# Kernel optimization log

Hardware: AMD Instinct MI355X
Metric: run time of the kernel (lower is better)

## Reference

```python
import jax, jax.numpy as jnp
import numpy as np
import math

B, L, D, H = 4, 4096, 1024, 16
d = D // H

def setup_inputs() -> dict:
    key = jax.random.key(0)
    ks = jax.random.split(key, 8)
    s = 0.02
    x = jax.random.normal(ks[0], (B, L, D), dtype=jnp.float32)
    Wqkv_w = jax.random.normal(ks[1], (3 * D, D), dtype=jnp.float32) * s
    Wqkv_b = jnp.zeros((3 * D,), dtype=jnp.float32)
    out_w = jax.random.normal(ks[2], (D, D), dtype=jnp.float32) * s
    out_b = jnp.zeros((D,), dtype=jnp.float32)
    W_static = jax.random.normal(ks[3], (H, d, d), dtype=jnp.float32) * s
    Lambda_raw = jax.random.uniform(ks[4], (H, d, d), dtype=jnp.float32, minval=-3.0, maxval=3.0)
    g = 0.5 / math.sqrt(d)
    Gamma = jax.random.uniform(ks[5], (H, d, d), dtype=jnp.float32, minval=-g, maxval=g)
    return {"x": x, "Wqkv_w": Wqkv_w, "Wqkv_b": Wqkv_b, "out_w": out_w,
            "out_b": out_b, "W_static": W_static, "Lambda_raw": Lambda_raw, "Gamma": Gamma}

def _stp_forward(x, Wqkv_w, Wqkv_b, out_w, out_b, W_static, Lambda_raw, Gamma):
    b, l, dm = x.shape
    scale = 1.0 / math.sqrt(d)
    qkv = x @ Wqkv_w.T + Wqkv_b                      # (B,L,3D)
    qkv = qkv.reshape(b, l, 3, H, d)                 # 'b l (three h d)'
    qkv = jnp.transpose(qkv, (2, 0, 3, 1, 4))        # (3,B,H,L,d)
    q, k, v = qkv[0], qkv[1], qkv[2]
    k = k * scale
    retention = 1.0 - jax.nn.sigmoid(Lambda_raw)     # (H,d,d)

    # scan over time: carry state (B,H,d,d)
    qs = jnp.moveaxis(q, 2, 0)                       # (L,B,H,d)
    ks_ = jnp.moveaxis(k, 2, 0)
    vs = jnp.moveaxis(v, 2, 0)

    def step(state, qkv_t):
        q_t, k_t, v_t = qkv_t                        # each (B,H,d)
        hebbian = jnp.einsum('bhi,bhj->bhij', v_t, k_t)
        state = retention[None] * state + Gamma[None] * hebbian
        y_t = jnp.einsum('bhij,bhj->bhi', W_static[None] + state, q_t)
        return state, y_t

    state0 = jnp.zeros((b, H, d, d), dtype=x.dtype)
    _, ys = jax.lax.scan(step, state0, (qs, ks_, vs))  # ys: (L,B,H,d)
    y = jnp.transpose(ys, (1, 0, 2, 3)).reshape(b, l, dm)  # 'b h l d -> b l (h d)'
    return y @ out_w.T + out_b

def reference(x, Wqkv_w, Wqkv_b, out_w, out_b, W_static, Lambda_raw, Gamma):
    return _stp_forward(x, Wqkv_w, Wqkv_b, out_w, out_b, W_static, Lambda_raw, Gamma)
```

## Files before the change

### kernel.cpp

```cpp
#include <hip/hip_runtime.h>
#include <stdint.h>

typedef unsigned short u16;
typedef __bf16 bf16x8 __attribute__((ext_vector_type(8)));
typedef float  f32x4  __attribute__((ext_vector_type(4)));

#define GLOBAL_AS __attribute__((address_space(1)))
#define LDS_AS    __attribute__((address_space(3)))

#define B_ 4
#define L_ 4096
#define D_ 1024
#define H_ 16
#define TD 3072

__device__ __forceinline__ float bf2f(u16 h) {
    union { uint32_t u; float f; } v; v.u = ((uint32_t)h) << 16; return v.f;
}
__device__ __forceinline__ u16 f2bf(float f) {
    union { float f; uint32_t u; } v; v.f = f;
    uint32_t u = v.u;
    u += 0x7fffu + ((u >> 16) & 1u);
    return (u16)(u >> 16);
}
__device__ __forceinline__ void unp2(uint32_t u, float* f) {
    union { uint32_t u; float f; } lo, hi;
    lo.u = u << 16; hi.u = u & 0xffff0000u;
    f[0] = lo.f; f[1] = hi.f;
}
__device__ __forceinline__ void unp8(uint4 u, float* f) {
    unp2(u.x, f); unp2(u.y, f + 2); unp2(u.z, f + 4); unp2(u.w, f + 6);
}

#define DPP_STEP(N)                                                           \
    {                                                                         \
        union { float f; int i; } s_, a_;                                     \
        a_.f = x;                                                             \
        s_.i = __builtin_amdgcn_update_dpp(0, a_.i, 0x110 + N, 0xf, 0xf, true); \
        x += s_.f;                                                            \
    }
__device__ __forceinline__ float grp_sum8(float x) {
    DPP_STEP(1) DPP_STEP(2) DPP_STEP(4)
    return x;
}

__device__ __forceinline__ uint4 ld8f(const float* p) {
    const float4 a = *(const float4*)p;
    const float4 b = *(const float4*)(p + 4);
    uint4 r;
    r.x = (uint32_t)f2bf(a.x) | ((uint32_t)f2bf(a.y) << 16);
    r.y = (uint32_t)f2bf(a.z) | ((uint32_t)f2bf(a.w) << 16);
    r.z = (uint32_t)f2bf(b.x) | ((uint32_t)f2bf(b.y) << 16);
    r.w = (uint32_t)f2bf(b.z) | ((uint32_t)f2bf(b.w) << 16);
    return r;
}

__device__ __forceinline__ void stc(u16* p, float v)   { *p = f2bf(v); }
__device__ __forceinline__ void stc(float* p, float v) { *p = v; }

__global__ __launch_bounds__(256) void cvt_f32_bf16(
    const float* __restrict__ in, u16* __restrict__ out, size_t n8)
{
    size_t i = (size_t)blockIdx.x * 256 + threadIdx.x;
    if (i >= n8) return;
    *(uint4*)(out + i * 8) = ld8f(in + i * 8);
}

template <typename TC>
__global__ __launch_bounds__(256) void gemm_bt_bias_bf16(
    const u16* __restrict__ A, const u16* __restrict__ W,
    const float* __restrict__ bias, TC* __restrict__ C,
    int M, int N, int K)
{
    __shared__ u16 As[128 * 32];
    __shared__ u16 Bs[128 * 32];

    const int tid  = threadIdx.x;
    const int lane = tid & 63;
    const int wid  = tid >> 6;
    const int bm = blockIdx.y * 128;
    const int bn = blockIdx.x * 128;

    const int wm = (wid & 1) * 64;
    const int wn = (wid >> 1) * 64;
    const int fr   = lane & 15;
    const int quad = lane >> 4;

    const u16* Ag = A + (size_t)(bm + (tid >> 2)) * K + (tid & 3) * 8;
    const u16* Wg = W + (size_t)(bn + (tid >> 2)) * K + (tid & 3) * 8;
    const size_t rskip = (size_t)64 * K;

    u16* AsW = As + wid * 512;
    u16* BsW = Bs + wid * 512;

    f32x4 acc[4][4] = {};

    for (int k0 = 0; k0 < K; k0 += 32) {
        __syncthreads();
        __builtin_amdgcn_global_load_lds((const GLOBAL_AS void*)(Ag + k0),
                                         (LDS_AS void*)(AsW),        16, 0, 0);
        __builtin_amdgcn_global_load_lds((const GLOBAL_AS void*)(Ag + rskip + k0),
                                         (LDS_AS void*)(AsW + 2048), 16, 0, 0);
        __builtin_amdgcn_global_load_lds((const GLOBAL_AS void*)(Wg + k0),
                                         (LDS_AS void*)(BsW),        16, 0, 0);
        __builtin_amdgcn_global_load_lds((const GLOBAL_AS void*)(Wg + rskip + k0),
                                         (LDS_AS void*)(BsW + 2048), 16, 0, 0);
        __syncthreads();

        bf16x8 af[4], bfv[4];
#pragma unroll
        for (int tm = 0; tm < 4; ++tm) {
            int m = wm + tm * 16 + fr;
            af[tm] = *(const bf16x8*)&As[m * 32 + quad * 8];
        }
#pragma unroll
        for (int tn = 0; tn < 4; ++tn) {
            int n = wn + tn * 16 + fr;
            bfv[tn] = *(const bf16x8*)&Bs[n * 32 + quad * 8];
        }
#pragma unroll
        for (int tm = 0; tm < 4; ++tm)
#pragma unroll
            for (int tn = 0; tn < 4; ++tn)
                acc[tm][tn] = __builtin_amdgcn_mfma_f32_16x16x32_bf16(
                    af[tm], bfv[tn], acc[tm][tn], 0, 0, 0);
    }

#pragma unroll
    for (int tm = 0; tm < 4; ++tm) {
#pragma unroll
        for (int tn = 0; tn < 4; ++tn) {
            const int col = bn + wn + tn * 16 + fr;
            const float bv = bias[col];
#pragma unroll
            for (int r = 0; r < 4; ++r) {
                const int row = bm + wm + tm * 16 + quad * 4 + r;
                stc(&C[(size_t)row * N + col], acc[tm][tn][r] + bv);
            }
        }
    }
}

__global__ __launch_bounds__(256, 4) void stp_scan_local(
    const u16* __restrict__ qkv, const float* __restrict__ Lam,
    const float* __restrict__ Gam, float* __restrict__ F,
    int nchunk, int tchunk)
{
    const int c = blockIdx.x, h = blockIdx.y, b = blockIdx.z;
    const int t = threadIdx.x;
    const int ig = t >> 3, jc = t & 7;
    const int i0 = ig << 1, j0 = jc << 3;
    const int hij = (h << 12) + (i0 << 6) + j0;

    float R2[2][8], RG[2][8], G[2][8], s[2][8];
#pragma unroll
    for (int r = 0; r < 2; ++r)
#pragma unroll
        for (int j = 0; j < 8; ++j) {
            const float Rv = 1.0f / (1.0f + expf(Lam[hij + r * 64 + j]));
            const float Gv = Gam[hij + r * 64 + j] * 0.125f;
            R2[r][j] = Rv * Rv;
            RG[r][j] = Rv * Gv;
            G[r][j]  = Gv;
            s[r][j]  = 0.0f;
        }

    const u16* rowp = qkv + (size_t)(b * L_ + c * tchunk) * TD;
    const int koff = D_ + (h << 6) + j0;
    const int voff = 2 * D_ + (h << 6) + i0;

    uint4    k0 = *(const uint4*)(rowp + koff);
    uint4    k1 = *(const uint4*)(rowp + TD + koff);
    uint32_t v0 = *(const uint32_t*)(rowp + voff);
    uint32_t v1 = *(const uint32_t*)(rowp + TD + voff);

    for (int tt = 0; tt < tchunk; tt += 2) {
        uint4    k0n = *(const uint4*)(rowp + 2 * TD + koff);
        uint4    k1n = *(const uint4*)(rowp + 3 * TD + koff);
        uint32_t v0n = *(const uint32_t*)(rowp + 2 * TD + voff);
        uint32_t v1n = *(const uint32_t*)(rowp + 3 * TD + voff);

        float kf0[8], kf1[8];
        unp8(k0, kf0); unp8(k1, kf1);
        const float a0 = bf2f((u16)v0), a1 = bf2f((u16)(v0 >> 16));
        const float b0 = bf2f((u16)v1), b1 = bf2f((u16)(v1 >> 16));
#pragma unroll
        for (int j = 0; j < 8; ++j) {
            s[0][j] = fmaf(R2[0][j], s[0][j],
                           fmaf(G[0][j], b0 * kf1[j], RG[0][j] * (a0 * kf0[j])));
            s[1][j] = fmaf(R2[1][j], s[1][j],
                           fmaf(G[1][j], b1 * kf1[j], RG[1][j] * (a1 * kf0[j])));
        }
        k0 = k0n; k1 = k1n; v0 = v0n; v1 = v1n;
        rowp += 2 * TD;
    }

    float* Fp = F + (((size_t)(b * H_ + h) * nchunk + c) << 12) + (i0 << 6) + j0;
#pragma unroll
    for (int r = 0; r < 2; ++r) {
        *(f32x4*)(Fp + r * 64)     = *(const f32x4*)(&s[r][0]);
        *(f32x4*)(Fp + r * 64 + 4) = *(const f32x4*)(&s[r][4]);
    }
}

__global__ __launch_bounds__(256) void stp_combine(
    const float* __restrict__ Lam, float* __restrict__ F,
    int nchunk, int tchunk)
{
    const int h = blockIdx.x, b = blockIdx.y;
    const int t = threadIdx.x;
    const int i = t >> 2, jc = t & 3, j0 = jc << 4;
    const int hij = (h << 12) + (i << 6) + j0;

    float Rt[16], s[16];
#pragma unroll
    for (int j = 0; j < 16; ++j) {
        float R = 1.0f / (1.0f + expf(Lam[hij + j]));
        Rt[j] = powf(R, (float)tchunk);
        s[j] = 0.0f;
    }
    float* base = F + (((size_t)(b * H_ + h) * nchunk) << 12) + (i << 6) + j0;
    for (int c = 0; c < nchunk; ++c) {
        float* p = base + ((size_t)c << 12);
        float tmp[16];
#pragma unroll
        for (int j = 0; j < 16; ++j) tmp[j] = p[j];
#pragma unroll
        for (int j = 0; j < 16; ++j) { p[j] = s[j]; s[j] = fmaf(Rt[j], s[j], tmp[j]); }
    }
}

__global__ __launch_bounds__(256, 4) void stp_scan_out(
    const u16* __restrict__ qkv, const float* __restrict__ Lam,
    const float* __restrict__ Gam, const float* __restrict__ Wst,
    const float* __restrict__ Sinit, u16* __restrict__ y,
    int nchunk, int tchunk)
{
    const int c = blockIdx.x, h = blockIdx.y, b = blockIdx.z;
    const int t = threadIdx.x;
    const int ig = t >> 3, jc = t & 7;
    const int i0 = ig << 1, j0 = jc << 3;
    const int hij = (h << 12) + (i0 << 6) + j0;

    float R[2][8], Gv[2][8], Cc[2][8], s[2][8];
    const float* Sp = Sinit + (((size_t)(b * H_ + h) * nchunk + c) << 12) + (i0 << 6) + j0;
#pragma unroll
    for (int r = 0; r < 2; ++r)
#pragma unroll
        for (int j = 0; j < 8; ++j) {
            const float Rv = 1.0f / (1.0f + expf(Lam[hij + r * 64 + j]));
            const float Wv = Wst[hij + r * 64 + j];
            R[r][j]  = Rv;
            Gv[r][j] = Gam[hij + r * 64 + j] * 0.125f;
            Cc[r][j] = Wv * (1.0f - Rv);
            s[r][j]  = Sp[r * 64 + j] + Wv;
        }

    const u16* rowp = qkv + (size_t)(b * L_ + c * tchunk) * TD;
    const int qoff = (h << 6) + j0;
    const int koff = D_ + qoff;
    const int voff = 2 * D_ + (h << 6) + i0;
    u16* yp = y + (size_t)(b * L_ + c * tchunk) * D_ + (h << 6) + i0;

    uint4    qu = *(const uint4*)(rowp + qoff);
    uint4    ku = *(const uint4*)(rowp + koff);
    uint32_t vu = *(const uint32_t*)(rowp + voff);

    for (int tt = 0; tt < tchunk; ++tt) {
        uint4    qn = *(const uint4*)(rowp + TD + qoff);
        uint4    kn = *(const uint4*)(rowp + TD + koff);
        uint32_t vn = *(const uint32_t*)(rowp + TD + voff);

        float qf[8], kf[8];
        unp8(qu, qf); unp8(ku, kf);
        const float v0 = bf2f((u16)vu);
        const float v1 = bf2f((u16)(vu >> 16));

        float ya0 = 0.0f, ya1 = 0.0f;
#pragma unroll
        for (int j = 0; j < 8; ++j) {
            s[0][j] = fmaf(R[0][j], s[0][j], fmaf(Gv[0][j] * v0, kf[j], Cc[0][j]));
            ya0 = fmaf(s[0][j], qf[j], ya0);
            s[1][j] = fmaf(R[1][j], s[1][j], fmaf(Gv[1][j] * v1, kf[j], Cc[1][j]));
            ya1 = fmaf(s[1][j], qf[j], ya1);
        }
        ya0 = grp_sum8(ya0);
        ya1 = grp_sum8(ya1);
        if ((t & 7) == 7) {
            uint32_t pk = (uint32_t)f2bf(ya0) | ((uint32_t)f2bf(ya1) << 16);
            *(uint32_t*)yp = pk;
        }
        qu = qn; ku = kn; vu = vn;
        rowp += TD; yp += D_;
    }
}

__global__ void zero_out_f32(float* p, size_t n) {
    size_t i = (size_t)blockIdx.x * blockDim.x + threadIdx.x;
    if (i < n) p[i] = 0.0f;
}

extern "C" void kernel_launch(void* const* d_in, const int* in_sizes, int n_in,
                              void* d_out, int out_size, void* d_ws, size_t ws_size,
                              hipStream_t stream)
{
    const float* x      = (const float*)d_in[0];
    const float* Wqkv_w = (const float*)d_in[1];
    const float* Wqkv_b = (const float*)d_in[2];
    const float* out_w  = (const float*)d_in[3];
    const float* out_b  = (const float*)d_in[4];
    const float* Wst    = (const float*)d_in[5];
    const float* Lam    = (const float*)d_in[6];
    const float* Gam    = (const float*)d_in[7];
    float* out = (float*)d_out;

    const size_t qkv_e = (size_t)B_ * L_ * TD;
    const size_t y_e   = (size_t)B_ * L_ * D_;
    const size_t fixed = qkv_e * 2 + y_e * 2;

    int nchunk = 32;
    size_t fbytes = (size_t)B_ * H_ * nchunk * 64 * 64 * 4;
    if (ws_size < fixed + fbytes) {
        nchunk = 16;
        fbytes = (size_t)B_ * H_ * nchunk * 64 * 64 * 4;
    }
    if (ws_size < fixed + fbytes) {
        zero_out_f32<<<(out_size + 255) / 256, 256, 0, stream>>>(out, (size_t)out_size);
        return;
    }
    const int tchunk = L_ / nchunk;

    u16*   qkv = (u16*)d_ws;
    u16*   y   = qkv + qkv_e;
    float* F   = (float*)(y + y_e);
    u16*   xb    = y;
    u16*   wqkvb = (u16*)F;
    u16*   outwb = (u16*)F;

    cvt_f32_bf16<<<(B_ * L_ * D_ / 8 + 255) / 256, 256, 0, stream>>>(
        x, xb, (size_t)B_ * L_ * D_ / 8);
    cvt_f32_bf16<<<(TD * D_ / 8 + 255) / 256, 256, 0, stream>>>(
        Wqkv_w, wqkvb, (size_t)TD * D_ / 8);
    gemm_bt_bias_bf16<u16><<<dim3(TD / 128, (B_ * L_) / 128), 256, 0, stream>>>(
        xb, wqkvb, Wqkv_b, qkv, B_ * L_, TD, D_);
    stp_scan_local<<<dim3(nchunk, H_, B_), 256, 0, stream>>>(
        qkv, Lam, Gam, F, nchunk, tchunk);
    stp_combine<<<dim3(H_, B_), 256, 0, stream>>>(Lam, F, nchunk, tchunk);
    stp_scan_out<<<dim3(nchunk, H_, B_), 256, 0, stream>>>(
        qkv, Lam, Gam, Wst, F, y, nchunk, tchunk);
    cvt_f32_bf16<<<(D_ * D_ / 8 + 255) / 256, 256, 0, stream>>>(
        out_w, outwb, (size_t)D_ * D_ / 8);
    gemm_bt_bias_bf16<float><<<dim3(D_ / 128, (B_ * L_) / 128), 256, 0, stream>>>(
        y, outwb, out_b, out, B_ * L_, D_, D_);
}
```

Before: 615.1 us.

## Double GEMM K-tile to 64 and swizzle workgroup order across XCDs

```diff
diff --git a/kernel.cpp b/kernel.cpp
--- a/kernel.cpp
+++ b/kernel.cpp
@@ -72,58 +72,68 @@
     const float* __restrict__ bias, TC* __restrict__ C,
     int M, int N, int K)
 {
-    __shared__ u16 As[128 * 32];
-    __shared__ u16 Bs[128 * 32];
+    __shared__ u16 As[128 * 64];
+    __shared__ u16 Bs[128 * 64];
 
     const int tid  = threadIdx.x;
     const int lane = tid & 63;
     const int wid  = tid >> 6;
-    const int bm = blockIdx.y * 128;
-    const int bn = blockIdx.x * 128;
+
+    const int nwg = gridDim.x * gridDim.y;
+    const int wg  = blockIdx.y * gridDim.x + blockIdx.x;
+    const int qq  = nwg >> 3;
+    const int swz = (wg & 7) * qq + (wg >> 3);
+    const int bm = (swz / gridDim.x) * 128;
+    const int bn = (swz % gridDim.x) * 128;
 
     const int wm = (wid & 1) * 64;
     const int wn = (wid >> 1) * 64;
     const int fr   = lane & 15;
     const int quad = lane >> 4;
 
-    const u16* Ag = A + (size_t)(bm + (tid >> 2)) * K + (tid & 3) * 8;
-    const u16* Wg = W + (size_t)(bn + (tid >> 2)) * K + (tid & 3) * 8;
-    const size_t rskip = (size_t)64 * K;
-
-    u16* AsW = As + wid * 512;
-    u16* BsW = Bs + wid * 512;
+    const int srow = (lane >> 3);
+    const int skg  = (lane & 7) * 8;
+    const u16* Ag = A + (size_t)(bm + wid * 8 + srow) * K + skg;
+    const u16* Wg = W + (size_t)(bn + wid * 8 + srow) * K + skg;
+
+    u16* AsW = As + (wid * 8) * 64;
+    u16* BsW = Bs + (wid * 8) * 64;
 
     f32x4 acc[4][4] = {};
 
-    for (int k0 = 0; k0 < K; k0 += 32) {
+    for (int k0 = 0; k0 < K; k0 += 64) {
         __syncthreads();
-        __builtin_amdgcn_global_load_lds((const GLOBAL_AS void*)(Ag + k0),
-                                         (LDS_AS void*)(AsW),        16, 0, 0);
-        __builtin_amdgcn_global_load_lds((const GLOBAL_AS void*)(Ag + rskip + k0),
-                                         (LDS_AS void*)(AsW + 2048), 16, 0, 0);
-        __builtin_amdgcn_global_load_lds((const GLOBAL_AS void*)(Wg + k0),
-                                         (LDS_AS void*)(BsW),        16, 0, 0);
-        __builtin_amdgcn_global_load_lds((const GLOBAL_AS void*)(Wg + rskip + k0),
-                                         (LDS_AS void*)(BsW + 2048), 16, 0, 0);
+#pragma unroll
+        for (int p = 0; p < 4; ++p) {
+            __builtin_amdgcn_global_load_lds(
+                (const GLOBAL_AS void*)(Ag + (size_t)(p * 32) * K + k0),
+                (LDS_AS void*)(AsW + p * 32 * 64), 16, 0, 0);
+            __builtin_amdgcn_global_load_lds(
+                (const GLOBAL_AS void*)(Wg + (size_t)(p * 32) * K + k0),
+                (LDS_AS void*)(BsW + p * 32 * 64), 16, 0, 0);
+        }
         __syncthreads();
 
-        bf16x8 af[4], bfv[4];
-#pragma unroll
-        for (int tm = 0; tm < 4; ++tm) {
-            int m = wm + tm * 16 + fr;
-            af[tm] = *(const bf16x8*)&As[m * 32 + quad * 8];
-        }
-#pragma unroll
-        for (int tn = 0; tn < 4; ++tn) {
-            int n = wn + tn * 16 + fr;
-            bfv[tn] = *(const bf16x8*)&Bs[n * 32 + quad * 8];
-        }
-#pragma unroll
-        for (int tm = 0; tm < 4; ++tm)
-#pragma unroll
-            for (int tn = 0; tn < 4; ++tn)
-                acc[tm][tn] = __builtin_amdgcn_mfma_f32_16x16x32_bf16(
-                    af[tm], bfv[tn], acc[tm][tn], 0, 0, 0);
+#pragma unroll
+        for (int ks = 0; ks < 2; ++ks) {
+            bf16x8 af[4], bfv[4];
+#pragma unroll
+            for (int tm = 0; tm < 4; ++tm) {
+                int m = wm + tm * 16 + fr;
+                af[tm] = *(const bf16x8*)&As[m * 64 + ks * 32 + quad * 8];
+            }
+#pragma unroll
+            for (int tn = 0; tn < 4; ++tn) {
+                int n = wn + tn * 16 + fr;
+                bfv[tn] = *(const bf16x8*)&Bs[n * 64 + ks * 32 + quad * 8];
+            }
+#pragma unroll
+            for (int tm = 0; tm < 4; ++tm)
+#pragma unroll
+                for (int tn = 0; tn < 4; ++tn)
+                    acc[tm][tn] = __builtin_amdgcn_mfma_f32_16x16x32_bf16(
+                        af[tm], bfv[tn], acc[tm][tn], 0, 0, 0);
+        }
     }
 
 #pragma unroll
```

After: 635.6 us. +3.3%, slower.
